# Performance work log

Measured on AMD Instinct MI355X. Metric: run time of the kernel, lower is better.

The kernel has to match this reference:

```python
import jax, jax.numpy as jnp
import numpy as np

N = 100000
E = 600000
H = 128
OUT = 64
L = 3

def glorot(key, shape):
    fan_in, fan_out = shape[0], shape[1]
    lim = jnp.sqrt(6.0 / (fan_in + fan_out))
    return jax.random.uniform(key, shape, jnp.float32, -lim, lim)

def setup_inputs() -> dict:
    key = jax.random.key(0)
    ks = jax.random.split(key, 20)
    x = jax.random.normal(ks[0], (N, H), jnp.float32)
    edge_index = jax.random.randint(ks[1], (2, E), 0, N, jnp.int64)
    edge_attr = jax.random.uniform(ks[2], (E, 1), jnp.float32)
    # stacked per-layer params [L, ...]
    W_lin = jnp.stack([glorot(jax.random.fold_in(ks[3], i), (H, H)) for i in range(L)])
    b_lin = jnp.zeros((L, H), jnp.float32)
    W_msg = jnp.stack([glorot(jax.random.fold_in(ks[4], i), (H + 1, H)) for i in range(L)])
    b_msg = jnp.zeros((L, H), jnp.float32)
    W_l = jnp.stack([glorot(jax.random.fold_in(ks[5], i), (H, H)) for i in range(L)])
    b_l = jnp.zeros((L, H), jnp.float32)
    W_r = jnp.stack([glorot(jax.random.fold_in(ks[6], i), (H, H)) for i in range(L)])
    W_dec = glorot(ks[7], (H, H))
    b_dec = jnp.zeros((H,), jnp.float32)
    W_fin = glorot(ks[8], (H, OUT))
    b_fin = jnp.zeros((OUT,), jnp.float32)
    return {"x": x, "edge_attr": edge_attr, "W_lin": W_lin, "b_lin": b_lin,
            "W_msg": W_msg, "b_msg": b_msg, "W_l": W_l, "b_l": b_l, "W_r": W_r,
            "W_dec": W_dec, "b_dec": b_dec, "W_fin": W_fin, "b_fin": b_fin,
            "edge_index": edge_index}

def reference(x, edge_attr, W_lin, b_lin, W_msg, b_msg, W_l, b_l, W_r,
              W_dec, b_dec, W_fin, b_fin, edge_index):
    src, dst = edge_index[0], edge_index[1]  # j -> i (source_to_target)
    # mean-aggregation denominator: in-degree clamped to 1
    deg = jax.ops.segment_sum(jnp.ones((E,), jnp.float32), dst, num_segments=N)
    inv_deg = (1.0 / jnp.maximum(deg, 1.0))[:, None]  # [N,1]
    for l in range(L):
        h = jax.nn.relu(x @ W_lin[l] + b_lin[l])          # [N,H]
        msg_in = jnp.concatenate([h[src], edge_attr], -1)  # [E,H+1]
        msg = jax.nn.relu(msg_in @ W_msg[l] + b_msg[l])    # [E,H]
        agg = jax.ops.segment_sum(msg, dst, num_segments=N) * inv_deg  # [N,H]
        out = (agg @ W_l[l] + b_l[l]) + x @ W_r[l]         # lin_l(agg) + lin_r(x_r)
        x = jax.nn.relu(out)  # dropout p=0.0 -> identity
    emb = jax.nn.relu(x @ W_dec + b_dec)
    logits = emb @ W_fin + b_fin  # [N,OUT]
    return logits
```

## Files before the change

### kernel.cpp

```cpp
#include <hip/hip_runtime.h>

using short8 = __attribute__((ext_vector_type(8))) short;
using f32x4  = __attribute__((ext_vector_type(4))) float;

constexpr int HD = 128;
constexpr int NBLK_SCAT = 2048;

__device__ __forceinline__ unsigned short f2bf(float f) {
    unsigned u = __builtin_bit_cast(unsigned, f);
    u += 0x7fffu + ((u >> 16) & 1u);
    return (unsigned short)(u >> 16);
}
__device__ __forceinline__ float bflo(unsigned u) { return __builtin_bit_cast(float, u << 16); }
__device__ __forceinline__ float bfhi(unsigned u) { return __builtin_bit_cast(float, u & 0xffff0000u); }

__device__ __forceinline__ short8 ldg8(const unsigned short* p) {
    return *reinterpret_cast<const short8*>(p);
}

template<int NC2, bool F32OUT>
__device__ __forceinline__ void dev_chain(unsigned short* As1, unsigned short* Hs,
    const unsigned short* __restrict__ A, const unsigned short* __restrict__ Wt1,
    const unsigned short* __restrict__ Wtc, const float* __restrict__ b1,
    const float* __restrict__ b2, void* __restrict__ Out, int nrows, int bid)
{
    const int tid  = threadIdx.x;
    const int lane = tid & 63, wave = tid >> 6;
    const int lr = lane & 15, lg = lane >> 4;
    const int row0 = bid * 64;

#pragma unroll
    for (int it = 0; it < 4; ++it) {
        const int q   = wave * 4 + it;
        const int c   = q * 64 + lane;
        const int row = c >> 4, cw = c & 15;
        int grow = row0 + row; grow = grow < nrows ? grow : nrows - 1;
        const int gco = (cw ^ (row & 7)) << 3;
        __builtin_amdgcn_global_load_lds((const unsigned int*)(A + (long)grow * HD + gco),
                                         (unsigned int*)&As1[q * 512], 16, 0, 0);
    }

    const int cb1 = wave * 32;
    short8 bf1[2][4];
#pragma unroll
    for (int ct = 0; ct < 2; ++ct) {
        const unsigned short* bp = Wt1 + (long)(cb1 + ct * 16 + lr) * HD + lg * 8;
#pragma unroll
        for (int kt = 0; kt < 4; ++kt) bf1[ct][kt] = ldg8(bp + kt * 32);
    }
    constexpr int CT2 = NC2 / 64;
    const int cb2 = wave * (NC2 / 4);
    short8 bfc[CT2][4];
#pragma unroll
    for (int ct = 0; ct < CT2; ++ct) {
        const unsigned short* bp = Wtc + (long)(cb2 + ct * 16 + lr) * HD + lg * 8;
#pragma unroll
        for (int kt = 0; kt < 4; ++kt) bfc[ct][kt] = ldg8(bp + kt * 32);
    }

    __syncthreads();

    f32x4 acc[4][2] = {};
#pragma unroll
    for (int kt = 0; kt < 4; ++kt) {
        short8 af[4];
#pragma unroll
        for (int rt = 0; rt < 4; ++rt)
            af[rt] = *reinterpret_cast<const short8*>(
                &As1[(rt * 16 + lr) * HD + (((kt * 4 + lg) ^ (lr & 7)) << 3)]);
#pragma unroll
        for (int rt = 0; rt < 4; ++rt)
#pragma unroll
            for (int ct = 0; ct < 2; ++ct)
                acc[rt][ct] = __builtin_amdgcn_mfma_f32_16x16x32_bf16(af[rt], bf1[ct][kt], acc[rt][ct], 0, 0, 0);
    }

    const float bv1[2] = { b1[cb1 + lr], b1[cb1 + 16 + lr] };
#pragma unroll
    for (int rt = 0; rt < 4; ++rt)
#pragma unroll
        for (int ct = 0; ct < 2; ++ct) {
            const int cc = cb1 + ct * 16 + lr;
#pragma unroll
            for (int i = 0; i < 4; ++i) {
                const int row = rt * 16 + lg * 4 + i;
                const float v = fmaxf(acc[rt][ct][i] + bv1[ct], 0.f);
                Hs[row * HD + ((((cc >> 3) ^ (row & 7)) << 3) | (cc & 7))] = f2bf(v);
            }
        }
    __syncthreads();

    f32x4 acc2[4][CT2] = {};
#pragma unroll
    for (int kt = 0; kt < 4; ++kt) {
        short8 ah[4];
#pragma unroll
        for (int rt = 0; rt < 4; ++rt)
            ah[rt] = *reinterpret_cast<const short8*>(
                &Hs[(rt * 16 + lr) * HD + (((kt * 4 + lg) ^ (lr & 7)) << 3)]);
#pragma unroll
        for (int rt = 0; rt < 4; ++rt)
#pragma unroll
            for (int ct = 0; ct < CT2; ++ct)
                acc2[rt][ct] = __builtin_amdgcn_mfma_f32_16x16x32_bf16(ah[rt], bfc[ct][kt], acc2[rt][ct], 0, 0, 0);
    }
    float bv2[CT2];
#pragma unroll
    for (int ct = 0; ct < CT2; ++ct) bv2[ct] = b2[cb2 + ct * 16 + lr];
#pragma unroll
    for (int rt = 0; rt < 4; ++rt)
#pragma unroll
        for (int ct = 0; ct < CT2; ++ct) {
            const int cc = cb2 + ct * 16 + lr;
#pragma unroll
            for (int i = 0; i < 4; ++i) {
                const int r = row0 + rt * 16 + lg * 4 + i;
                if (r < nrows) {
                    const float v = acc2[rt][ct][i] + bv2[ct];
                    if constexpr (F32OUT) ((float*)Out)[(long)r * NC2 + cc] = v;
                    else ((unsigned short*)Out)[(long)r * NC2 + cc] = f2bf(v);
                }
            }
        }
}

template<int NC2, bool F32OUT>
__global__ __launch_bounds__(256)
void k_chain(const unsigned short* __restrict__ A, const unsigned short* __restrict__ Wt1,
             const unsigned short* __restrict__ Wtc, const float* __restrict__ b1,
             const float* __restrict__ b2, void* __restrict__ Out, int nrows)
{
    __shared__ __align__(16) unsigned short As1[64 * HD];
    __shared__ __align__(16) unsigned short Hs [64 * HD];
    dev_chain<NC2, F32OUT>(As1, Hs, A, Wt1, Wtc, b1, b2, Out, nrows, blockIdx.x);
}

__global__ __launch_bounds__(256)
void k_dual(const unsigned short* __restrict__ A1, const unsigned short* __restrict__ Wt1,
            const unsigned short* __restrict__ A2, const unsigned short* __restrict__ Wt2,
            const float* __restrict__ bias, unsigned short* __restrict__ Out, int nrows)
{
    __shared__ __align__(16) unsigned short As1[64 * HD];
    __shared__ __align__(16) unsigned short As2[64 * HD];

    const int tid  = threadIdx.x;
    const int lane = tid & 63, wave = tid >> 6;
    const int lr = lane & 15, lg = lane >> 4;
    const int row0 = blockIdx.x * 64;

#pragma unroll
    for (int it = 0; it < 4; ++it) {
        const int q   = wave * 4 + it;
        const int c   = q * 64 + lane;
        const int row = c >> 4, cw = c & 15;
        int grow = row0 + row; grow = grow < nrows ? grow : nrows - 1;
        const int gco = (cw ^ (row & 7)) << 3;
        __builtin_amdgcn_global_load_lds((const unsigned int*)(A1 + (long)grow * HD + gco),
                                         (unsigned int*)&As1[q * 512], 16, 0, 0);
        __builtin_amdgcn_global_load_lds((const unsigned int*)(A2 + (long)grow * HD + gco),
                                         (unsigned int*)&As2[q * 512], 16, 0, 0);
    }

    const int cb = wave * 32;
    short8 bf1[2][4], bf2[2][4];
#pragma unroll
    for (int ct = 0; ct < 2; ++ct) {
        const unsigned short* p1 = Wt1 + (long)(cb + ct * 16 + lr) * HD + lg * 8;
        const unsigned short* p2 = Wt2 + (long)(cb + ct * 16 + lr) * HD + lg * 8;
#pragma unroll
        for (int kt = 0; kt < 4; ++kt) { bf1[ct][kt] = ldg8(p1 + kt * 32); bf2[ct][kt] = ldg8(p2 + kt * 32); }
    }

    __syncthreads();

    f32x4 acc[4][2] = {};
#pragma unroll
    for (int kt = 0; kt < 4; ++kt) {
        short8 af[4], ag[4];
#pragma unroll
        for (int rt = 0; rt < 4; ++rt) {
            const int base = (rt * 16 + lr) * HD + (((kt * 4 + lg) ^ (lr & 7)) << 3);
            af[rt] = *reinterpret_cast<const short8*>(&As1[base]);
            ag[rt] = *reinterpret_cast<const short8*>(&As2[base]);
        }
#pragma unroll
        for (int rt = 0; rt < 4; ++rt)
#pragma unroll
            for (int ct = 0; ct < 2; ++ct) {
                acc[rt][ct] = __builtin_amdgcn_mfma_f32_16x16x32_bf16(af[rt], bf1[ct][kt], acc[rt][ct], 0, 0, 0);
                acc[rt][ct] = __builtin_amdgcn_mfma_f32_16x16x32_bf16(ag[rt], bf2[ct][kt], acc[rt][ct], 0, 0, 0);
            }
    }

    const float bv[2] = { bias[cb + lr], bias[cb + 16 + lr] };
#pragma unroll
    for (int rt = 0; rt < 4; ++rt)
#pragma unroll
        for (int ct = 0; ct < 2; ++ct) {
            const int cc = cb + ct * 16 + lr;
#pragma unroll
            for (int i = 0; i < 4; ++i) {
                const int r = row0 + rt * 16 + lg * 4 + i;
                if (r < nrows) Out[(long)r * HD + cc] = f2bf(fmaxf(acc[rt][ct][i] + bv[ct], 0.f));
            }
        }
}

__global__ __launch_bounds__(256)
void k_dualdec(const unsigned short* __restrict__ Agg, const unsigned short* __restrict__ X,
               const unsigned short* __restrict__ WtL, const unsigned short* __restrict__ WtR,
               const float* __restrict__ bl_, const unsigned short* __restrict__ Wdec,
               const float* __restrict__ bdec, const unsigned short* __restrict__ Wfin,
               const float* __restrict__ bfin, float* __restrict__ Out, int n)
{
    __shared__ __align__(16) unsigned short Ag[64 * HD];
    __shared__ __align__(16) unsigned short Xs[64 * HD];
    __shared__ __align__(16) unsigned short Ts[64 * HD];

    const int tid  = threadIdx.x;
    const int lane = tid & 63, wave = tid >> 6;
    const int lr = lane & 15, lg = lane >> 4;
    const int row0 = blockIdx.x * 64;

#pragma unroll
    for (int it = 0; it < 4; ++it) {
        const int q   = wave * 4 + it;
        const int c   = q * 64 + lane;
        const int row = c >> 4, cw = c & 15;
        int grow = row0 + row; grow = grow < n ? grow : n - 1;
        const int gco = (cw ^ (row & 7)) << 3;
        __builtin_amdgcn_global_load_lds((const unsigned int*)(Agg + (long)grow * HD + gco),
                                         (unsigned int*)&Ag[q * 512], 16, 0, 0);
        __builtin_amdgcn_global_load_lds((const unsigned int*)(X + (long)grow * HD + gco),
                                         (unsigned int*)&Xs[q * 512], 16, 0, 0);
    }

    const int cb = wave * 32;
    short8 bl[2][4], br[2][4];
#pragma unroll
    for (int ct = 0; ct < 2; ++ct) {
        const unsigned short* pl = WtL + (long)(cb + ct * 16 + lr) * HD + lg * 8;
        const unsigned short* pr = WtR + (long)(cb + ct * 16 + lr) * HD + lg * 8;
#pragma unroll
        for (int kt = 0; kt < 4; ++kt) { bl[ct][kt] = ldg8(pl + kt * 32); br[ct][kt] = ldg8(pr + kt * 32); }
    }
    __syncthreads();

    {
        f32x4 acc[4][2] = {};
#pragma unroll
        for (int kt = 0; kt < 4; ++kt) {
            short8 aa[4], ax[4];
#pragma unroll
            for (int rt = 0; rt < 4; ++rt) {
                const int base = (rt * 16 + lr) * HD + (((kt * 4 + lg) ^ (lr & 7)) << 3);
                aa[rt] = *reinterpret_cast<const short8*>(&Ag[base]);
                ax[rt] = *reinterpret_cast<const short8*>(&Xs[base]);
            }
#pragma unroll
            for (int rt = 0; rt < 4; ++rt)
#pragma unroll
                for (int ct = 0; ct < 2; ++ct) {
                    acc[rt][ct] = __builtin_amdgcn_mfma_f32_16x16x32_bf16(aa[rt], bl[ct][kt], acc[rt][ct], 0, 0, 0);
                    acc[rt][ct] = __builtin_amdgcn_mfma_f32_16x16x32_bf16(ax[rt], br[ct][kt], acc[rt][ct], 0, 0, 0);
                }
        }
        const float bv[2] = { bl_[cb + lr], bl_[cb + 16 + lr] };
#pragma unroll
        for (int rt = 0; rt < 4; ++rt)
#pragma unroll
            for (int ct = 0; ct < 2; ++ct) {
                const int cc = cb + ct * 16 + lr;
#pragma unroll
                for (int i = 0; i < 4; ++i) {
                    const int row = rt * 16 + lg * 4 + i;
                    const float v = fmaxf(acc[rt][ct][i] + bv[ct], 0.f);
                    Ts[row * HD + ((((cc >> 3) ^ (row & 7)) << 3) | (cc & 7))] = f2bf(v);
                }
            }
    }
    __syncthreads();

    {
        short8 bd[2][4];
#pragma unroll
        for (int ct = 0; ct < 2; ++ct) {
            const unsigned short* bp = Wdec + (long)(cb + ct * 16 + lr) * HD + lg * 8;
#pragma unroll
            for (int kt = 0; kt < 4; ++kt) bd[ct][kt] = ldg8(bp + kt * 32);
        }
        f32x4 acc[4][2] = {};
#pragma unroll
        for (int kt = 0; kt < 4; ++kt) {
            short8 ah[4];
#pragma unroll
            for (int rt = 0; rt < 4; ++rt)
                ah[rt] = *reinterpret_cast<const short8*>(
                    &Ts[(rt * 16 + lr) * HD + (((kt * 4 + lg) ^ (lr & 7)) << 3)]);
#pragma unroll
            for (int rt = 0; rt < 4; ++rt)
#pragma unroll
                for (int ct = 0; ct < 2; ++ct)
                    acc[rt][ct] = __builtin_amdgcn_mfma_f32_16x16x32_bf16(ah[rt], bd[ct][kt], acc[rt][ct], 0, 0, 0);
        }
        const float bv[2] = { bdec[cb + lr], bdec[cb + 16 + lr] };
#pragma unroll
        for (int rt = 0; rt < 4; ++rt)
#pragma unroll
            for (int ct = 0; ct < 2; ++ct) {
                const int cc = cb + ct * 16 + lr;
#pragma unroll
                for (int i = 0; i < 4; ++i) {
                    const int row = rt * 16 + lg * 4 + i;
                    const float v = fmaxf(acc[rt][ct][i] + bv[ct], 0.f);
                    Ag[row * HD + ((((cc >> 3) ^ (row & 7)) << 3) | (cc & 7))] = f2bf(v);
                }
            }
    }
    __syncthreads();

    {
        const int cbf = wave * 16;
        short8 bfn[4];
#pragma unroll
        for (int kt = 0; kt < 4; ++kt)
            bfn[kt] = ldg8(Wfin + (long)(cbf + lr) * HD + lg * 8 + kt * 32);
        f32x4 acc[4] = {};
#pragma unroll
        for (int kt = 0; kt < 4; ++kt) {
            short8 ah[4];
#pragma unroll
            for (int rt = 0; rt < 4; ++rt)
                ah[rt] = *reinterpret_cast<const short8*>(
                    &Ag[(rt * 16 + lr) * HD + (((kt * 4 + lg) ^ (lr & 7)) << 3)]);
#pragma unroll
            for (int rt = 0; rt < 4; ++rt)
                acc[rt] = __builtin_amdgcn_mfma_f32_16x16x32_bf16(ah[rt], bfn[kt], acc[rt], 0, 0, 0);
        }
        const float bv = bfin[cbf + lr];
#pragma unroll
        for (int rt = 0; rt < 4; ++rt)
#pragma unroll
            for (int i = 0; i < 4; ++i) {
                const int r = row0 + rt * 16 + lg * 4 + i;
                if (r < n) Out[(long)r * 64 + cbf + lr] = acc[rt][i] + bv;
            }
    }
}

__device__ __forceinline__ void dev_deg(const int* __restrict__ dst, int* __restrict__ deg,
                                        int nE, int n, int bid, int nblk) {
    const int grp = bid & 7, bin = bid >> 3, nbin = nblk >> 3;
    const int chunk = (n + 7) >> 3;
    const int lo = grp * chunk, hi = min(n, lo + chunk);
    for (int e = bin * 256 + threadIdx.x; e < nE; e += nbin * 256) {
        const int d = dst[e];
        if (d >= lo && d < hi) atomicAdd(&deg[d], 1);
    }
}

__device__ __forceinline__ void dev_fill(const int* __restrict__ src, const int* __restrict__ dst,
                                         const float* __restrict__ eattr, const int* __restrict__ rowstart,
                                         int* __restrict__ degcur, uint2* __restrict__ csr_rec,
                                         int nE, int n, int bid, int nblk) {
    const int grp = bid & 7, bin = bid >> 3, nbin = nblk >> 3;
    const int chunk = (n + 7) >> 3;
    const int lo = grp * chunk, hi = min(n, lo + chunk);
    for (int e = bin * 256 + threadIdx.x; e < nE; e += nbin * 256) {
        const int d = dst[e];
        if (d >= lo && d < hi) {
            const int p = rowstart[d] + atomicSub(&degcur[d], 1) - 1;
            uint2 rec;
            rec.x = (unsigned)src[e];
            rec.y = __builtin_bit_cast(unsigned, eattr[e]);
            csr_rec[p] = rec;
        }
    }
}

__global__ __launch_bounds__(256)
void k_u1(const int* __restrict__ dst, int* __restrict__ deg, int nE,
          const float* __restrict__ xin, unsigned short* __restrict__ xb, long n8, int ncast,
          const float* __restrict__ Wlin, const float* __restrict__ Wmsg,
          const float* __restrict__ Wl,   const float* __restrict__ Wr,
          const float* __restrict__ Wdec, const float* __restrict__ Wfin,
          unsigned short* __restrict__ wt, int n)
{
    const int bid = blockIdx.x;
    if (bid < NBLK_SCAT) { dev_deg(dst, deg, nE, n, bid, NBLK_SCAT); return; }
    const int b = bid - NBLK_SCAT;
    if (b < ncast) {
        const long i = (long)b * 256 + threadIdx.x;
        if (i >= n8) return;
        const float4 v0 = *((const float4*)xin + i * 2);
        const float4 v1 = *((const float4*)xin + i * 2 + 1);
        unsigned o[4];
        o[0] = (unsigned)f2bf(v0.x) | ((unsigned)f2bf(v0.y) << 16);
        o[1] = (unsigned)f2bf(v0.z) | ((unsigned)f2bf(v0.w) << 16);
        o[2] = (unsigned)f2bf(v1.x) | ((unsigned)f2bf(v1.y) << 16);
        o[3] = (unsigned)f2bf(v1.z) | ((unsigned)f2bf(v1.w) << 16);
        *(uint4*)(xb + i * 8) = *(uint4*)o;
        return;
    }
    const int local = b - ncast;
    const int m = local >> 6;
    const float* src; int C = 128;
    if      (m < 3)  src = Wlin + m * 16384;
    else if (m < 6)  src = Wmsg + (m - 3) * (129 * 128);
    else if (m < 9)  src = Wl   + (m - 6) * 16384;
    else if (m < 12) src = Wr   + (m - 9) * 16384;
    else if (m == 12) src = Wdec;
    else { src = Wfin; C = 64; }
    const int elems = C * 128;
    const int e = (local & 63) * 256 + threadIdx.x;
    if (e >= elems) return;
    const int c = e >> 7, k = e & 127;
    wt[m * 16384 + e] = f2bf(src[k * C + c]);
}

__global__ __launch_bounds__(256)
void k_u2(const int* __restrict__ src, const int* __restrict__ dst,
          const float* __restrict__ eattr, const int* __restrict__ rowstart,
          int* __restrict__ degcur, uint2* __restrict__ csr_rec, int nE,
          const unsigned short* __restrict__ A, const unsigned short* __restrict__ Wt1,
          const unsigned short* __restrict__ Wtc, const float* __restrict__ b1,
          const float* __restrict__ b2, unsigned short* __restrict__ Out, int n)
{
    __shared__ __align__(16) unsigned short As1[64 * HD];
    __shared__ __align__(16) unsigned short Hs [64 * HD];
    if (blockIdx.x < NBLK_SCAT) {
        dev_fill(src, dst, eattr, rowstart, degcur, csr_rec, nE, n, blockIdx.x, NBLK_SCAT);
        return;
    }
    dev_chain<128, false>(As1, Hs, A, Wt1, Wtc, b1, b2, Out, n, blockIdx.x - NBLK_SCAT);
}

__global__ void k_chunksum(const int* __restrict__ deg, int* __restrict__ csum, int n) {
    __shared__ int s[256];
    int t = threadIdx.x, i = blockIdx.x * 256 + t;
    s[t] = (i < n) ? deg[i] : 0;
    __syncthreads();
    for (int o = 128; o > 0; o >>= 1) { if (t < o) s[t] += s[t + o]; __syncthreads(); }
    if (t == 0) csum[blockIdx.x] = s[0];
}

__global__ void k_scanmid(const int* __restrict__ csum, int* __restrict__ cbase,
                          int* __restrict__ rowstart, int nch, int n) {
    __shared__ int s[512];
    int t = threadIdx.x;
    int v = (t < nch) ? csum[t] : 0;
    s[t] = v; __syncthreads();
    for (int off = 1; off < 512; off <<= 1) {
        int tmp = (t >= off) ? s[t - off] : 0;
        __syncthreads();
        s[t] += tmp;
        __syncthreads();
    }
    if (t < nch) cbase[t] = s[t] - v;
    if (t == nch - 1) rowstart[n] = s[t];
}

__global__ void k_scan2(const int* __restrict__ deg, const int* __restrict__ cbase,
                        int* __restrict__ rowstart, float* __restrict__ inv_deg, int n) {
    __shared__ int s[256];
    int t = threadIdx.x, i = blockIdx.x * 256 + t;
    int v = (i < n) ? deg[i] : 0;
    s[t] = v; __syncthreads();
    for (int off = 1; off < 256; off <<= 1) {
        int tmp = (t >= off) ? s[t - off] : 0;
        __syncthreads();
        s[t] += tmp;
        __syncthreads();
    }
    if (i < n) {
        rowstart[i] = cbase[blockIdx.x] + s[t] - v;
        inv_deg[i] = 1.0f / fmaxf((float)v, 1.0f);
    }
}

__global__ __launch_bounds__(256)
void k_agg(const unsigned short* __restrict__ g, const uint2* __restrict__ rec,
           const int* __restrict__ rs, const float* __restrict__ inv_deg,
           const float* __restrict__ wlast, unsigned short* __restrict__ agg, int n) {
    const int lane = threadIdx.x & 15;
    const int node = blockIdx.x * 16 + (threadIdx.x >> 4);
    if (node >= n) return;
    const int c0 = lane * 8;
    const float4 wla = *(const float4*)(wlast + c0);
    const float4 wlb = *(const float4*)(wlast + c0 + 4);
    const int p0 = rs[node], p1 = rs[node + 1];
    float a0=0,a1=0,a2=0,a3=0,a4=0,a5=0,a6=0,a7=0;
    int p = p0;
    for (; p + 4 <= p1; p += 4) {
        uint2 r[4];
#pragma unroll
        for (int u = 0; u < 4; ++u) r[u] = rec[p + u];
        uint4 G[4];
#pragma unroll
        for (int u = 0; u < 4; ++u) G[u] = *(const uint4*)(g + (long)r[u].x * HD + c0);
#pragma unroll
        for (int u = 0; u < 4; ++u) {
            const float e = __builtin_bit_cast(float, r[u].y);
            a0 += fmaxf(fmaf(e, wla.x, bflo(G[u].x)), 0.f);
            a1 += fmaxf(fmaf(e, wla.y, bfhi(G[u].x)), 0.f);
            a2 += fmaxf(fmaf(e, wla.z, bflo(G[u].y)), 0.f);
            a3 += fmaxf(fmaf(e, wla.w, bfhi(G[u].y)), 0.f);
            a4 += fmaxf(fmaf(e, wlb.x, bflo(G[u].z)), 0.f);
            a5 += fmaxf(fmaf(e, wlb.y, bfhi(G[u].z)), 0.f);
            a6 += fmaxf(fmaf(e, wlb.z, bflo(G[u].w)), 0.f);
            a7 += fmaxf(fmaf(e, wlb.w, bfhi(G[u].w)), 0.f);
        }
    }
    for (; p < p1; ++p) {
        const uint2 r0 = rec[p];
        const float e0 = __builtin_bit_cast(float, r0.y);
        const uint4 G0 = *(const uint4*)(g + (long)r0.x * HD + c0);
        a0 += fmaxf(fmaf(e0, wla.x, bflo(G0.x)), 0.f);
        a1 += fmaxf(fmaf(e0, wla.y, bfhi(G0.x)), 0.f);
        a2 += fmaxf(fmaf(e0, wla.z, bflo(G0.y)), 0.f);
        a3 += fmaxf(fmaf(e0, wla.w, bfhi(G0.y)), 0.f);
        a4 += fmaxf(fmaf(e0, wlb.x, bflo(G0.z)), 0.f);
        a5 += fmaxf(fmaf(e0, wlb.y, bfhi(G0.z)), 0.f);
        a6 += fmaxf(fmaf(e0, wlb.z, bflo(G0.w)), 0.f);
        a7 += fmaxf(fmaf(e0, wlb.w, bfhi(G0.w)), 0.f);
    }
    const float id = inv_deg[node];
    uint4 o;
    o.x = (unsigned)f2bf(a0 * id) | ((unsigned)f2bf(a1 * id) << 16);
    o.y = (unsigned)f2bf(a2 * id) | ((unsigned)f2bf(a3 * id) << 16);
    o.z = (unsigned)f2bf(a4 * id) | ((unsigned)f2bf(a5 * id) << 16);
    o.w = (unsigned)f2bf(a6 * id) | ((unsigned)f2bf(a7 * id) << 16);
    *(uint4*)(agg + (long)node * HD + c0) = o;
}

extern "C" void kernel_launch(void* const* d_in, const int* in_sizes, int n_in,
                              void* d_out, int out_size, void* d_ws, size_t ws_size,
                              hipStream_t stream)
{
    const float* x     = (const float*)d_in[0];
    const float* eattr = (const float*)d_in[1];
    const float* W_lin = (const float*)d_in[2];
    const float* b_lin = (const float*)d_in[3];
    const float* W_msg = (const float*)d_in[4];
    const float* b_msg = (const float*)d_in[5];
    const float* W_l   = (const float*)d_in[6];
    const float* b_l   = (const float*)d_in[7];
    const float* W_r   = (const float*)d_in[8];
    const float* W_dec = (const float*)d_in[9];
    const float* b_dec = (const float*)d_in[10];
    const float* W_fin = (const float*)d_in[11];
    const float* b_fin = (const float*)d_in[12];
    const int*   ei    = (const int*)d_in[13];

    const int N = in_sizes[0] / HD;
    const int E = in_sizes[1];
    const int* srcv = ei;
    const int* dstv = ei + E;

    char* wsb = (char*)d_ws;
    size_t off = 0;
    auto carve = [&](size_t bytes) -> void* {
        void* p = wsb + off;
        off += (bytes + 255) & ~(size_t)255;
        return p;
    };
    unsigned short* xb = (unsigned short*)carve((size_t)N * HD * 2);
    unsigned short* t1 = (unsigned short*)carve((size_t)N * HD * 2);
    unsigned short* t2 = (unsigned short*)carve((size_t)N * HD * 2);
    unsigned short* t3 = (unsigned short*)carve((size_t)N * HD * 2);
    unsigned short* wt = (unsigned short*)carve((size_t)14 * 16384 * 2);
    uint2* csr_rec  = (uint2*)carve((size_t)E * 8);
    int*   rowstart = (int*)carve((size_t)(N + 1) * 4);
    int*   deg      = (int*)carve((size_t)N * 4);
    float* inv_deg  = (float*)carve((size_t)N * 4);
    const int NCH = (N + 255) / 256;
    int* csum  = (int*)carve((size_t)NCH * 4);
    int* cbase = (int*)carve((size_t)NCH * 4);

    if (off > ws_size) {
        hipMemsetAsync(d_out, 0, (size_t)out_size * 4, stream);
        return;
    }

    hipMemsetAsync(deg, 0, (size_t)N * 4, stream);

    auto WT = [&](int m) { return wt + (size_t)m * 16384; };
    const int NB64 = (N + 63) / 64;
    const int GAGG = (N + 15) / 16;
    const long n8 = (long)N * HD / 8;
    const int ncast = (int)((n8 + 255) / 256);

    k_u1<<<NBLK_SCAT + ncast + 14 * 64, 256, 0, stream>>>(
        dstv, deg, E, x, xb, n8, ncast, W_lin, W_msg, W_l, W_r, W_dec, W_fin, wt, N);
    k_chunksum<<<NCH, 256, 0, stream>>>(deg, csum, N);
    k_scanmid<<<1, 512, 0, stream>>>(csum, cbase, rowstart, NCH, N);
    k_scan2<<<NCH, 256, 0, stream>>>(deg, cbase, rowstart, inv_deg, N);

    k_u2<<<NBLK_SCAT + NB64, 256, 0, stream>>>(
        srcv, dstv, eattr, rowstart, deg, csr_rec, E,
        xb, WT(0), WT(3), b_lin, b_msg, t2, N);

    auto wlast = [&](int l) { return W_msg + (size_t)l * (HD + 1) * HD + (size_t)HD * HD; };

    k_agg<<<GAGG, 256, 0, stream>>>(t2, csr_rec, rowstart, inv_deg, wlast(0), t1, N);
    k_dual<<<NB64, 256, 0, stream>>>(t1, WT(6), xb, WT(9), b_l, t2, N);
    k_chain<128, false><<<NB64, 256, 0, stream>>>(t2, WT(1), WT(4), b_lin + HD, b_msg + HD, t3, N);
    k_agg<<<GAGG, 256, 0, stream>>>(t3, csr_rec, rowstart, inv_deg, wlast(1), t1, N);
    k_dual<<<NB64, 256, 0, stream>>>(t1, WT(7), t2, WT(10), b_l + HD, t3, N);
    k_chain<128, false><<<NB64, 256, 0, stream>>>(t3, WT(2), WT(5), b_lin + 2 * HD, b_msg + 2 * HD, t2, N);
    k_agg<<<GAGG, 256, 0, stream>>>(t2, csr_rec, rowstart, inv_deg, wlast(2), t1, N);
    k_dualdec<<<NB64, 256, 0, stream>>>(t1, t3, WT(8), WT(11), b_l + 2 * HD,
                                        WT(12), b_dec, WT(13), b_fin, (float*)d_out, N);
}
```

Baseline: 340.2 us.

## Fuse dual SAGE update with next layer's lin/msg chain into one kernel

Merges k_dual (lin_l(agg)+lin_r(x), relu) and the following k_chain (lin, then the message linear) into a single k_dualchain kernel. The freshly computed node features stay in LDS for the chain GEMMs instead of being re-read from global memory, and one launch per layer goes away. The X buffer is updated in place; this is safe only because each block reads its own rows into LDS before writing them back. LDS use grows to three 64x128 tiles per block, which may reduce occupancy.

```diff
diff --git a/kernel.cpp b/kernel.cpp
--- a/kernel.cpp
+++ b/kernel.cpp
@@ -124,24 +124,17 @@
         }
 }
 
-template<int NC2, bool F32OUT>
 __global__ __launch_bounds__(256)
-void k_chain(const unsigned short* __restrict__ A, const unsigned short* __restrict__ Wt1,
-             const unsigned short* __restrict__ Wtc, const float* __restrict__ b1,
-             const float* __restrict__ b2, void* __restrict__ Out, int nrows)
+void k_dualchain(const unsigned short* __restrict__ Agg, const unsigned short* __restrict__ X,
+                 const unsigned short* __restrict__ WtL, const unsigned short* __restrict__ WtR,
+                 const float* __restrict__ bl_,
+                 const unsigned short* __restrict__ Wt1, const float* __restrict__ b1,
+                 const unsigned short* __restrict__ Wtc, const float* __restrict__ b2,
+                 unsigned short* __restrict__ Xout, unsigned short* __restrict__ Gout, int n)
 {
-    __shared__ __align__(16) unsigned short As1[64 * HD];
-    __shared__ __align__(16) unsigned short Hs [64 * HD];
-    dev_chain<NC2, F32OUT>(As1, Hs, A, Wt1, Wtc, b1, b2, Out, nrows, blockIdx.x);
-}
-
-__global__ __launch_bounds__(256)
-void k_dual(const unsigned short* __restrict__ A1, const unsigned short* __restrict__ Wt1,
-            const unsigned short* __restrict__ A2, const unsigned short* __restrict__ Wt2,
-            const float* __restrict__ bias, unsigned short* __restrict__ Out, int nrows)
-{
-    __shared__ __align__(16) unsigned short As1[64 * HD];
-    __shared__ __align__(16) unsigned short As2[64 * HD];
+    __shared__ __align__(16) unsigned short Ag[64 * HD];
+    __shared__ __align__(16) unsigned short Xs[64 * HD];
+    __shared__ __align__(16) unsigned short Ts[64 * HD];
 
     const int tid  = threadIdx.x;
     const int lane = tid & 63, wave = tid >> 6;
@@ -153,57 +146,136 @@
         const int q   = wave * 4 + it;
         const int c   = q * 64 + lane;
         const int row = c >> 4, cw = c & 15;
-        int grow = row0 + row; grow = grow < nrows ? grow : nrows - 1;
+        int grow = row0 + row; grow = grow < n ? grow : n - 1;
         const int gco = (cw ^ (row & 7)) << 3;
-        __builtin_amdgcn_global_load_lds((const unsigned int*)(A1 + (long)grow * HD + gco),
-                                         (unsigned int*)&As1[q * 512], 16, 0, 0);
-        __builtin_amdgcn_global_load_lds((const unsigned int*)(A2 + (long)grow * HD + gco),
-                                         (unsigned int*)&As2[q * 512], 16, 0, 0);
+        __builtin_amdgcn_global_load_lds((const unsigned int*)(Agg + (long)grow * HD + gco),
+                                         (unsigned int*)&Ag[q * 512], 16, 0, 0);
+        __builtin_amdgcn_global_load_lds((const unsigned int*)(X + (long)grow * HD + gco),
+                                         (unsigned int*)&Xs[q * 512], 16, 0, 0);
     }
 
     const int cb = wave * 32;
-    short8 bf1[2][4], bf2[2][4];
+    short8 bl[2][4], br[2][4];
 #pragma unroll
     for (int ct = 0; ct < 2; ++ct) {
-        const unsigned short* p1 = Wt1 + (long)(cb + ct * 16 + lr) * HD + lg * 8;
-        const unsigned short* p2 = Wt2 + (long)(cb + ct * 16 + lr) * HD + lg * 8;
-#pragma unroll
-        for (int kt = 0; kt < 4; ++kt) { bf1[ct][kt] = ldg8(p1 + kt * 32); bf2[ct][kt] = ldg8(p2 + kt * 32); }
-    }
-
-    __syncthreads();
-
-    f32x4 acc[4][2] = {};
-#pragma unroll
-    for (int kt = 0; kt < 4; ++kt) {
-        short8 af[4], ag[4];
-#pragma unroll
-        for (int rt = 0; rt < 4; ++rt) {
-            const int base = (rt * 16 + lr) * HD + (((kt * 4 + lg) ^ (lr & 7)) << 3);
-            af[rt] = *reinterpret_cast<const short8*>(&As1[base]);
-            ag[rt] = *reinterpret_cast<const short8*>(&As2[base]);
-        }
+        const unsigned short* pl = WtL + (long)(cb + ct * 16 + lr) * HD + lg * 8;
+        const unsigned short* pr = WtR + (long)(cb + ct * 16 + lr) * HD + lg * 8;
+#pragma unroll
+        for (int kt = 0; kt < 4; ++kt) { bl[ct][kt] = ldg8(pl + kt * 32); br[ct][kt] = ldg8(pr + kt * 32); }
+    }
+    __syncthreads();
+
+    {
+        f32x4 acc[4][2] = {};
+#pragma unroll
+        for (int kt = 0; kt < 4; ++kt) {
+            short8 aa[4], ax[4];
+#pragma unroll
+            for (int rt = 0; rt < 4; ++rt) {
+                const int base = (rt * 16 + lr) * HD + (((kt * 4 + lg) ^ (lr & 7)) << 3);
+                aa[rt] = *reinterpret_cast<const short8*>(&Ag[base]);
+                ax[rt] = *reinterpret_cast<const short8*>(&Xs[base]);
+            }
+#pragma unroll
+            for (int rt = 0; rt < 4; ++rt)
+#pragma unroll
+                for (int ct = 0; ct < 2; ++ct) {
+                    acc[rt][ct] = __builtin_amdgcn_mfma_f32_16x16x32_bf16(aa[rt], bl[ct][kt], acc[rt][ct], 0, 0, 0);
+                    acc[rt][ct] = __builtin_amdgcn_mfma_f32_16x16x32_bf16(ax[rt], br[ct][kt], acc[rt][ct], 0, 0, 0);
+                }
+        }
+        const float bv[2] = { bl_[cb + lr], bl_[cb + 16 + lr] };
 #pragma unroll
         for (int rt = 0; rt < 4; ++rt)
 #pragma unroll
             for (int ct = 0; ct < 2; ++ct) {
-                acc[rt][ct] = __builtin_amdgcn_mfma_f32_16x16x32_bf16(af[rt], bf1[ct][kt], acc[rt][ct], 0, 0, 0);
-                acc[rt][ct] = __builtin_amdgcn_mfma_f32_16x16x32_bf16(ag[rt], bf2[ct][kt], acc[rt][ct], 0, 0, 0);
-            }
-    }
-
-    const float bv[2] = { bias[cb + lr], bias[cb + 16 + lr] };
-#pragma unroll
-    for (int rt = 0; rt < 4; ++rt)
+                const int cc = cb + ct * 16 + lr;
+#pragma unroll
+                for (int i = 0; i < 4; ++i) {
+                    const int row = rt * 16 + lg * 4 + i;
+                    const int r = row0 + row;
+                    const float v = fmaxf(acc[rt][ct][i] + bv[ct], 0.f);
+                    const unsigned short vb = f2bf(v);
+                    Ts[row * HD + ((((cc >> 3) ^ (row & 7)) << 3) | (cc & 7))] = vb;
+                    if (r < n) Xout[(long)r * HD + cc] = vb;
+                }
+            }
+    }
+    __syncthreads();
+
+    {
+        short8 b1f[2][4];
 #pragma unroll
         for (int ct = 0; ct < 2; ++ct) {
-            const int cc = cb + ct * 16 + lr;
-#pragma unroll
-            for (int i = 0; i < 4; ++i) {
-                const int r = row0 + rt * 16 + lg * 4 + i;
-                if (r < nrows) Out[(long)r * HD + cc] = f2bf(fmaxf(acc[rt][ct][i] + bv[ct], 0.f));
-            }
-        }
+            const unsigned short* bp = Wt1 + (long)(cb + ct * 16 + lr) * HD + lg * 8;
+#pragma unroll
+            for (int kt = 0; kt < 4; ++kt) b1f[ct][kt] = ldg8(bp + kt * 32);
+        }
+        f32x4 acc[4][2] = {};
+#pragma unroll
+        for (int kt = 0; kt < 4; ++kt) {
+            short8 ah[4];
+#pragma unroll
+            for (int rt = 0; rt < 4; ++rt)
+                ah[rt] = *reinterpret_cast<const short8*>(
+                    &Ts[(rt * 16 + lr) * HD + (((kt * 4 + lg) ^ (lr & 7)) << 3)]);
+#pragma unroll
+            for (int rt = 0; rt < 4; ++rt)
+#pragma unroll
+                for (int ct = 0; ct < 2; ++ct)
+                    acc[rt][ct] = __builtin_amdgcn_mfma_f32_16x16x32_bf16(ah[rt], b1f[ct][kt], acc[rt][ct], 0, 0, 0);
+        }
+        const float bv[2] = { b1[cb + lr], b1[cb + 16 + lr] };
+#pragma unroll
+        for (int rt = 0; rt < 4; ++rt)
+#pragma unroll
+            for (int ct = 0; ct < 2; ++ct) {
+                const int cc = cb + ct * 16 + lr;
+#pragma unroll
+                for (int i = 0; i < 4; ++i) {
+                    const int row = rt * 16 + lg * 4 + i;
+                    const float v = fmaxf(acc[rt][ct][i] + bv[ct], 0.f);
+                    Ag[row * HD + ((((cc >> 3) ^ (row & 7)) << 3) | (cc & 7))] = f2bf(v);
+                }
+            }
+    }
+    __syncthreads();
+
+    {
+        short8 bcf[2][4];
+#pragma unroll
+        for (int ct = 0; ct < 2; ++ct) {
+            const unsigned short* bp = Wtc + (long)(cb + ct * 16 + lr) * HD + lg * 8;
+#pragma unroll
+            for (int kt = 0; kt < 4; ++kt) bcf[ct][kt] = ldg8(bp + kt * 32);
+        }
+        f32x4 acc[4][2] = {};
+#pragma unroll
+        for (int kt = 0; kt < 4; ++kt) {
+            short8 ah[4];
+#pragma unroll
+            for (int rt = 0; rt < 4; ++rt)
+                ah[rt] = *reinterpret_cast<const short8*>(
+                    &Ag[(rt * 16 + lr) * HD + (((kt * 4 + lg) ^ (lr & 7)) << 3)]);
+#pragma unroll
+            for (int rt = 0; rt < 4; ++rt)
+#pragma unroll
+                for (int ct = 0; ct < 2; ++ct)
+                    acc[rt][ct] = __builtin_amdgcn_mfma_f32_16x16x32_bf16(ah[rt], bcf[ct][kt], acc[rt][ct], 0, 0, 0);
+        }
+        const float bv[2] = { b2[cb + lr], b2[cb + 16 + lr] };
+#pragma unroll
+        for (int rt = 0; rt < 4; ++rt)
+#pragma unroll
+            for (int ct = 0; ct < 2; ++ct) {
+                const int cc = cb + ct * 16 + lr;
+#pragma unroll
+                for (int i = 0; i < 4; ++i) {
+                    const int r = row0 + rt * 16 + lg * 4 + i;
+                    if (r < n) Gout[(long)r * HD + cc] = f2bf(acc[rt][ct][i] + bv[ct]);
+                }
+            }
+    }
 }
 
 __global__ __launch_bounds__(256)
@@ -603,12 +675,12 @@
     auto wlast = [&](int l) { return W_msg + (size_t)l * (HD + 1) * HD + (size_t)HD * HD; };
 
     k_agg<<<GAGG, 256, 0, stream>>>(t2, csr_rec, rowstart, inv_deg, wlast(0), t1, N);
-    k_dual<<<NB64, 256, 0, stream>>>(t1, WT(6), xb, WT(9), b_l, t2, N);
-    k_chain<128, false><<<NB64, 256, 0, stream>>>(t2, WT(1), WT(4), b_lin + HD, b_msg + HD, t3, N);
-    k_agg<<<GAGG, 256, 0, stream>>>(t3, csr_rec, rowstart, inv_deg, wlast(1), t1, N);
-    k_dual<<<NB64, 256, 0, stream>>>(t1, WT(7), t2, WT(10), b_l + HD, t3, N);
-    k_chain<128, false><<<NB64, 256, 0, stream>>>(t3, WT(2), WT(5), b_lin + 2 * HD, b_msg + 2 * HD, t2, N);
-    k_agg<<<GAGG, 256, 0, stream>>>(t2, csr_rec, rowstart, inv_deg, wlast(2), t1, N);
-    k_dualdec<<<NB64, 256, 0, stream>>>(t1, t3, WT(8), WT(11), b_l + 2 * HD,
+    k_dualchain<<<NB64, 256, 0, stream>>>(
+        t1, xb, WT(6), WT(9), b_l, WT(1), b_lin + HD, WT(4), b_msg + HD, t3, t2, N);
+    k_agg<<<GAGG, 256, 0, stream>>>(t2, csr_rec, rowstart, inv_deg, wlast(1), t1, N);
+    k_dualchain<<<NB64, 256, 0, stream>>>(
+        t1, t3, WT(7), WT(10), b_l + HD, WT(2), b_lin + 2 * HD, WT(5), b_msg + 2 * HD, t3, t1, N);
+    k_agg<<<GAGG, 256, 0, stream>>>(t1, csr_rec, rowstart, inv_deg, wlast(2), t2, N);
+    k_dualdec<<<NB64, 256, 0, stream>>>(t2, t3, WT(8), WT(11), b_l + 2 * HD,
                                         WT(12), b_dec, WT(13), b_fin, (float*)d_out, N);
 }
```

Result: faster. 326.6 us (-4.0%).
